# Optimization experiments

Measured on AMD Instinct MI355X. Metric: run time of the kernel, lower is better.

## Reference

```python
import jax, jax.numpy as jnp
import numpy as np

VOCAB = 32000
EMB = 256
HID = 512
SEQ = 512
SOS = 1  # word2vec key_to_index['<SOS>']; PAD assumed index 0 and never sampled


def setup_inputs() -> dict:
    key = jax.random.key(0)
    ks = jax.random.split(key, 8)
    k_lstm = 1.0 / np.sqrt(HID)
    k_out = 1.0 / np.sqrt(HID)
    return {
        # token ids in [2, VOCAB) so the PAD-skip branch never triggers
        "input_seq": jax.random.randint(ks[0], (1, SEQ), 2, VOCAB, dtype=jnp.int32),
        "h0": jnp.zeros((1, 1, HID), jnp.float32),
        "c0": jnp.zeros((1, 1, HID), jnp.float32),
        "embedding": jax.random.normal(ks[1], (VOCAB, EMB), jnp.float32) * 0.02,
        "W_ih": jax.random.uniform(ks[2], (4 * HID, EMB), jnp.float32, -k_lstm, k_lstm),
        "W_hh": jax.random.uniform(ks[3], (4 * HID, HID), jnp.float32, -k_lstm, k_lstm),
        "b_ih": jax.random.uniform(ks[4], (4 * HID,), jnp.float32, -k_lstm, k_lstm),
        "b_hh": jax.random.uniform(ks[5], (4 * HID,), jnp.float32, -k_lstm, k_lstm),
        "W_out": jax.random.uniform(ks[6], (VOCAB, HID), jnp.float32, -k_out, k_out),
        "b_out": jax.random.uniform(ks[7], (VOCAB,), jnp.float32, -k_out, k_out),
    }


def reference(input_seq, h0, c0, embedding, W_ih, W_hh, b_ih, b_hh, W_out, b_out):
    # tokens actually fed to the LSTM: <SOS> then the full teacher-forced sequence
    tokens = jnp.concatenate([jnp.array([SOS], jnp.int32), input_seq[0]])  # [S+1]
    emb = embedding[tokens]  # [S+1, E]
    bias = b_ih + b_hh

    def cell(carry, x_t):
        h, c = carry  # [H], [H]
        gates = W_ih @ x_t + W_hh @ h + bias  # [4H], torch gate order i,f,g,o
        i, f, g, o = jnp.split(gates, 4)
        i = jax.nn.sigmoid(i)
        f = jax.nn.sigmoid(f)
        g = jnp.tanh(g)
        o = jax.nn.sigmoid(o)
        c_new = f * c + i * g
        h_new = o * jnp.tanh(c_new)
        return (h_new, c_new), h_new

    (hT, cT), hs = jax.lax.scan(cell, (h0[0, 0], c0[0, 0]), emb)  # hs: [S+1, H]
    logits = hs @ W_out.T + b_out  # [S+1, V] (same math as per-step Linear + cat)
    outputs = logits[None]  # [1, S+1, V]
    return outputs, hT[None, None], cT[None, None]
```

## Files before the change

kernel.cpp:

```cpp
#include <hip/hip_runtime.h>
#include <cmath>

#define VOCAB 32000
#define EMB   256
#define HID   512
#define TLEN  513
#define G4    2048
#define NWG   32
#define SOS   1

typedef unsigned long long u64;
typedef unsigned int uivec4 __attribute__((ext_vector_type(4)));
typedef float f32x4 __attribute__((ext_vector_type(4)));
typedef short bf16x8 __attribute__((ext_vector_type(8)));

__device__ inline float fsig(float x)  { return __builtin_amdgcn_rcpf(1.f + __expf(-x)); }
__device__ inline float ftanh(float x) { return 1.f - 2.f * __builtin_amdgcn_rcpf(__expf(2.f * x) + 1.f); }
__device__ inline float fma4(f32x4 w, f32x4 h, float a) {
    return fmaf(w[0], h[0], fmaf(w[1], h[1], fmaf(w[2], h[2], fmaf(w[3], h[3], a))));
}

__device__ inline void bf16split(float f, short& h, short& l) {
    unsigned u = __float_as_uint(f);
    unsigned r = u + (0x7fffu + ((u >> 16) & 1u));
    unsigned hb = r & 0xffff0000u;
    h = (short)(hb >> 16);
    float res = f - __uint_as_float(hb);
    unsigned u2 = __float_as_uint(res);
    unsigned r2 = u2 + (0x7fffu + ((u2 >> 16) & 1u));
    l = (short)(r2 >> 16);
}

__global__ __launch_bounds__(256) void precompute_gates(
    const int* __restrict__ seq, const float* __restrict__ emb,
    const float* __restrict__ W_ih, const float* __restrict__ b_ih,
    const float* __restrict__ b_hh, float* __restrict__ Xg)
{
    __shared__ __align__(16) float ebuf[16][EMB];
    const int bt = blockIdx.x;
    const int br = blockIdx.y;
    const int tid = threadIdx.x;

    for (int tt = 0; tt < 16; ++tt) {
        int t = bt * 16 + tt;
        if (t < TLEN) {
            int tok = (t == 0) ? SOS : seq[t - 1];
            ebuf[tt][tid] = emb[(size_t)tok * EMB + tid];
        }
    }
    __syncthreads();

    const int row = br * 256 + tid;
    float acc[16];
#pragma unroll
    for (int tt = 0; tt < 16; ++tt) acc[tt] = 0.f;

    const float4* wp = (const float4*)(W_ih + (size_t)row * EMB);
#pragma unroll 4
    for (int k4 = 0; k4 < EMB / 4; ++k4) {
        float4 w = wp[k4];
#pragma unroll
        for (int tt = 0; tt < 16; ++tt) {
            float4 e = *(const float4*)&ebuf[tt][k4 * 4];
            acc[tt] = fmaf(w.x, e.x, fmaf(w.y, e.y, fmaf(w.z, e.z, fmaf(w.w, e.w, acc[tt]))));
        }
    }

    const float bias = b_ih[row] + b_hh[row];
    for (int tt = 0; tt < 16; ++tt) {
        int t = bt * 16 + tt;
        if (t < TLEN) Xg[(size_t)t * G4 + row] = acc[tt] + bias;
    }
}

__global__ __launch_bounds__(256, 1) void lstm_recurrence(
    const float* __restrict__ Xg, const float* __restrict__ W_hh,
    const float* __restrict__ h0, const float* __restrict__ c0,
    float* __restrict__ hs, u64* pk,
    float* __restrict__ out_hT, float* __restrict__ out_cT)
{
    __shared__ __align__(16) float hbuf[HID];
    __shared__ float pbuf[2][256];

    const int wg  = blockIdx.x;
    const int tid = threadIdx.x;
    const int wv  = tid >> 6;
    const int ln  = tid & 63;
    const int q   = ln >> 4;
    const int j   = ln & 15;
    const int row = q * HID + wg * 16 + j;

    f32x4 wreg[32];
    const f32x4* wp = (const f32x4*)(W_hh + (size_t)row * HID + wv * 128);
#pragma unroll
    for (int i = 0; i < 32; ++i) wreg[i] = wp[i];

    float c = (tid < 16) ? c0[wg * 16 + tid] : 0.f;
    {
        float2 h2 = *(const float2*)&h0[tid * 2];
        hbuf[tid * 2]     = h2.x;
        hbuf[tid * 2 + 1] = h2.y;
    }
    __syncthreads();

    for (int t = 0; t < TLEN; ++t) {
        float xg0 = 0.f, xg1 = 0.f, xg2 = 0.f, xg3 = 0.f;
        if (tid < 16) {
            const float* xp = Xg + (size_t)t * G4 + wg * 16 + tid;
            xg0 = xp[0]; xg1 = xp[512]; xg2 = xp[1024]; xg3 = xp[1536];
        }

        if (t > 0) {
            const unsigned tt = (unsigned)t;
            u64 sa = (u64)(uintptr_t)(pk + (size_t)(t & 1) * HID + 2 * tid);
            uivec4 r;
            do {
                asm volatile("global_load_dwordx4 %0, %1, off sc0 sc1\n\t"
                             "s_waitcnt vmcnt(0)" : "=v"(r) : "v"(sa));
            } while (r.y != tt || r.w != tt);
            hbuf[2 * tid]     = __uint_as_float(r.x);
            hbuf[2 * tid + 1] = __uint_as_float(r.z);
            asm volatile("s_waitcnt lgkmcnt(0)" ::: "memory");
        }

        float a0 = 0.f, a1 = 0.f, a2 = 0.f, a3 = 0.f;
        float a4 = 0.f, a5 = 0.f, a6 = 0.f, a7 = 0.f;
        const f32x4* hp = (const f32x4*)&hbuf[wv * 128];
#pragma unroll
        for (int i = 0; i < 32; i += 8) {
            a0 = fma4(wreg[i],     hp[i],     a0);
            a1 = fma4(wreg[i + 1], hp[i + 1], a1);
            a2 = fma4(wreg[i + 2], hp[i + 2], a2);
            a3 = fma4(wreg[i + 3], hp[i + 3], a3);
            a4 = fma4(wreg[i + 4], hp[i + 4], a4);
            a5 = fma4(wreg[i + 5], hp[i + 5], a5);
            a6 = fma4(wreg[i + 6], hp[i + 6], a6);
            a7 = fma4(wreg[i + 7], hp[i + 7], a7);
        }
        pbuf[t & 1][tid] = ((a0 + a1) + (a2 + a3)) + ((a4 + a5) + (a6 + a7));
        __syncthreads();

        if (tid < 16) {
            const float* pb = pbuf[t & 1];
            float gi = pb[tid]      + pb[64 + tid]  + pb[128 + tid] + pb[192 + tid] + xg0;
            float gf = pb[16 + tid] + pb[80 + tid]  + pb[144 + tid] + pb[208 + tid] + xg1;
            float gg = pb[32 + tid] + pb[96 + tid]  + pb[160 + tid] + pb[224 + tid] + xg2;
            float go = pb[48 + tid] + pb[112 + tid] + pb[176 + tid] + pb[240 + tid] + xg3;
            float i_ = fsig(gi);
            float f_ = fsig(gf);
            float g_ = ftanh(gg);
            float o_ = fsig(go);
            c = fmaf(f_, c, i_ * g_);
            float h_ = o_ * ftanh(c);
            if (t < TLEN - 1) {
                u64 word = ((u64)(unsigned)(t + 1) << 32) | (u64)__float_as_uint(h_);
                (void)__hip_atomic_exchange(
                    &pk[(size_t)((t + 1) & 1) * HID + wg * 16 + tid], word,
                    __ATOMIC_RELAXED, __HIP_MEMORY_SCOPE_AGENT);
            } else {
                out_hT[wg * 16 + tid] = h_;
                out_cT[wg * 16 + tid] = c;
            }
            hs[(size_t)t * HID + wg * 16 + tid] = h_;
        }
    }
}

#define GLDT 40

__global__ __launch_bounds__(256, 2) void out_gemm_mfma(
    const float* __restrict__ hs, const float* __restrict__ W_out,
    const float* __restrict__ b_out, float* __restrict__ out)
{
    __shared__ __align__(16) short Ah[128][GLDT];
    __shared__ __align__(16) short Al[128][GLDT];
    __shared__ __align__(16) short Bh[128][GLDT];
    __shared__ __align__(16) short Bl[128][GLDT];

    const int tb = blockIdx.x;
    const int vb = blockIdx.y;
    const int tid = threadIdx.x;
    const int w   = tid >> 6;
    const int l   = tid & 63;
    const int l15 = l & 15;
    const int lg  = l >> 4;
    const int m0 = tb * 128, n0 = vb * 128;

    const int sr = tid >> 1;
    const int kh = (tid & 1) * 16;

    f32x4 acc[2][8];
#pragma unroll
    for (int s = 0; s < 2; ++s)
#pragma unroll
        for (int cc = 0; cc < 8; ++cc) acc[s][cc] = (f32x4){0.f, 0.f, 0.f, 0.f};

    for (int k0 = 0; k0 < HID; k0 += 32) {
        {
            int trow = m0 + sr;
            float4 fa0 = make_float4(0.f,0.f,0.f,0.f), fa1 = fa0, fa2 = fa0, fa3 = fa0;
            if (trow < TLEN) {
                const float4* ap = (const float4*)(hs + (size_t)trow * HID + k0 + kh);
                fa0 = ap[0]; fa1 = ap[1]; fa2 = ap[2]; fa3 = ap[3];
            }
            float fv[16] = { fa0.x,fa0.y,fa0.z,fa0.w, fa1.x,fa1.y,fa1.z,fa1.w,
                             fa2.x,fa2.y,fa2.z,fa2.w, fa3.x,fa3.y,fa3.z,fa3.w };
#pragma unroll
            for (int g = 0; g < 2; ++g) {
                union { short s[8]; bf16x8 v; } ph, pl;
#pragma unroll
                for (int e = 0; e < 8; ++e) bf16split(fv[g * 8 + e], ph.s[e], pl.s[e]);
                *(bf16x8*)&Ah[sr][kh + 8 * g] = ph.v;
                *(bf16x8*)&Al[sr][kh + 8 * g] = pl.v;
            }
        }
        {
            const float4* bp = (const float4*)(W_out + (size_t)(n0 + sr) * HID + k0 + kh);
            float4 fb0 = bp[0], fb1 = bp[1], fb2 = bp[2], fb3 = bp[3];
            float fv[16] = { fb0.x,fb0.y,fb0.z,fb0.w, fb1.x,fb1.y,fb1.z,fb1.w,
                             fb2.x,fb2.y,fb2.z,fb2.w, fb3.x,fb3.y,fb3.z,fb3.w };
#pragma unroll
            for (int g = 0; g < 2; ++g) {
                union { short s[8]; bf16x8 v; } ph, pl;
#pragma unroll
                for (int e = 0; e < 8; ++e) bf16split(fv[g * 8 + e], ph.s[e], pl.s[e]);
                *(bf16x8*)&Bh[sr][kh + 8 * g] = ph.v;
                *(bf16x8*)&Bl[sr][kh + 8 * g] = pl.v;
            }
        }
        __syncthreads();

        bf16x8 ah[2], al2[2];
#pragma unroll
        for (int s = 0; s < 2; ++s) {
            ah[s]  = *(const bf16x8*)&Ah[32 * w + 16 * s + l15][8 * lg];
            al2[s] = *(const bf16x8*)&Al[32 * w + 16 * s + l15][8 * lg];
        }
#pragma unroll
        for (int cc = 0; cc < 8; ++cc) {
            bf16x8 bh = *(const bf16x8*)&Bh[16 * cc + l15][8 * lg];
            bf16x8 bl = *(const bf16x8*)&Bl[16 * cc + l15][8 * lg];
#pragma unroll
            for (int s = 0; s < 2; ++s) {
                acc[s][cc] = __builtin_amdgcn_mfma_f32_16x16x32_bf16(ah[s],  bh, acc[s][cc], 0, 0, 0);
                acc[s][cc] = __builtin_amdgcn_mfma_f32_16x16x32_bf16(ah[s],  bl, acc[s][cc], 0, 0, 0);
                acc[s][cc] = __builtin_amdgcn_mfma_f32_16x16x32_bf16(al2[s], bh, acc[s][cc], 0, 0, 0);
            }
        }
        __syncthreads();
    }

#pragma unroll
    for (int cc = 0; cc < 8; ++cc) {
        int col = n0 + 16 * cc + l15;
        float bo = b_out[col];
#pragma unroll
        for (int s = 0; s < 2; ++s) {
            int rbase = m0 + 32 * w + 16 * s + lg * 4;
#pragma unroll
            for (int r = 0; r < 4; ++r) {
                int trow = rbase + r;
                if (trow < TLEN) out[(size_t)trow * VOCAB + col] = acc[s][cc][r] + bo;
            }
        }
    }
}

extern "C" void kernel_launch(void* const* d_in, const int* in_sizes, int n_in,
                              void* d_out, int out_size, void* d_ws, size_t ws_size,
                              hipStream_t stream)
{
    const int*   seq   = (const int*)  d_in[0];
    const float* h0    = (const float*)d_in[1];
    const float* c0    = (const float*)d_in[2];
    const float* emb   = (const float*)d_in[3];
    const float* W_ih  = (const float*)d_in[4];
    const float* W_hh  = (const float*)d_in[5];
    const float* b_ih  = (const float*)d_in[6];
    const float* b_hh  = (const float*)d_in[7];
    const float* W_out = (const float*)d_in[8];
    const float* b_out = (const float*)d_in[9];

    float* out_logits = (float*)d_out;
    float* out_hT     = out_logits + (size_t)TLEN * VOCAB;
    float* out_cT     = out_hT + HID;

    float* Xg = (float*)d_ws;
    float* hs = Xg + (size_t)TLEN * G4;
    u64*   pk = (u64*)(hs + (size_t)TLEN * HID);

    (void)hipMemsetAsync(pk, 0, 2 * HID * sizeof(u64), stream);
    precompute_gates<<<dim3(33, 8), 256, 0, stream>>>(seq, emb, W_ih, b_ih, b_hh, Xg);
    lstm_recurrence<<<NWG, 256, 0, stream>>>(Xg, W_hh, h0, c0, hs, pk, out_hT, out_cT);
    out_gemm_mfma<<<dim3(5, 250), 256, 0, stream>>>(hs, W_out, b_out, out_logits);
}
```

Measured before the change: 957.4 us.

## Pre-split W_out into bf16 hi/lo in fused precompute kernel, feed MFMA gemm

Adds conversion blocks to the gate-precompute kernel that split W_out into bf16 high/low arrays in workspace. The recurrence also emits bf16 hi/lo copies of h. A new output GEMM loads the presplit operands directly instead of converting fp32 tiles inside the inner loop. The pk memset is folded into the fused kernel. The cost is extra memory traffic to write and reread the split weights.

```diff
diff --git a/kernel.cpp b/kernel.cpp
--- a/kernel.cpp
+++ b/kernel.cpp
@@ -8,6 +8,8 @@
 #define G4    2048
 #define NWG   32
 #define SOS   1
+#define NPRE  264
+#define NCVT  4000
 
 typedef unsigned long long u64;
 typedef unsigned int uivec4 __attribute__((ext_vector_type(4)));
@@ -31,15 +33,42 @@
     l = (short)(r2 >> 16);
 }
 
-__global__ __launch_bounds__(256) void precompute_gates(
+__global__ __launch_bounds__(256) void pre_fused(
     const int* __restrict__ seq, const float* __restrict__ emb,
     const float* __restrict__ W_ih, const float* __restrict__ b_ih,
-    const float* __restrict__ b_hh, float* __restrict__ Xg)
+    const float* __restrict__ b_hh, const float* __restrict__ W_out,
+    float* __restrict__ Xg, u64* pk,
+    short* __restrict__ Wh, short* __restrict__ Wl, int do_split)
 {
     __shared__ __align__(16) float ebuf[16][EMB];
-    const int bt = blockIdx.x;
-    const int br = blockIdx.y;
+    const int b   = blockIdx.x;
     const int tid = threadIdx.x;
+
+    if (b >= NPRE) {
+        if (!do_split) return;
+        if (b == NPRE) {
+#pragma unroll
+            for (int i = 0; i < 4; ++i) pk[tid + 256 * i] = 0;
+        }
+        const size_t base = (size_t)(b - NPRE) * 4096 + (size_t)tid * 16;
+        const float4* src = (const float4*)(W_out + base);
+        float4 f0 = src[0], f1 = src[1], f2 = src[2], f3 = src[3];
+        float fv[16] = { f0.x,f0.y,f0.z,f0.w, f1.x,f1.y,f1.z,f1.w,
+                         f2.x,f2.y,f2.z,f2.w, f3.x,f3.y,f3.z,f3.w };
+        union { short s[8]; bf16x8 v; } h0_, h1_, l0_, l1_;
+#pragma unroll
+        for (int e = 0; e < 8; ++e) bf16split(fv[e],     h0_.s[e], l0_.s[e]);
+#pragma unroll
+        for (int e = 0; e < 8; ++e) bf16split(fv[8 + e], h1_.s[e], l1_.s[e]);
+        *(bf16x8*)&Wh[base]     = h0_.v;
+        *(bf16x8*)&Wh[base + 8] = h1_.v;
+        *(bf16x8*)&Wl[base]     = l0_.v;
+        *(bf16x8*)&Wl[base + 8] = l1_.v;
+        return;
+    }
+
+    const int bt = b % 33;
+    const int br = b / 33;
 
     for (int tt = 0; tt < 16; ++tt) {
         int t = bt * 16 + tt;
@@ -76,8 +105,8 @@
 __global__ __launch_bounds__(256, 1) void lstm_recurrence(
     const float* __restrict__ Xg, const float* __restrict__ W_hh,
     const float* __restrict__ h0, const float* __restrict__ c0,
-    float* __restrict__ hs, u64* pk,
-    float* __restrict__ out_hT, float* __restrict__ out_cT)
+    float* __restrict__ hs, short* __restrict__ hs_h, short* __restrict__ hs_l,
+    u64* pk, float* __restrict__ out_hT, float* __restrict__ out_cT)
 {
     __shared__ __align__(16) float hbuf[HID];
     __shared__ float pbuf[2][256];
@@ -162,11 +191,104 @@
                 out_cT[wg * 16 + tid] = c;
             }
             hs[(size_t)t * HID + wg * 16 + tid] = h_;
+            short hh, hl; bf16split(h_, hh, hl);
+            hs_h[(size_t)t * HID + wg * 16 + tid] = hh;
+            hs_l[(size_t)t * HID + wg * 16 + tid] = hl;
         }
     }
 }
 
 #define GLDT 40
+
+__global__ __launch_bounds__(256, 2) void out_gemm_pre(
+    const short* __restrict__ hs_h, const short* __restrict__ hs_l,
+    const short* __restrict__ Wh, const short* __restrict__ Wl,
+    const float* __restrict__ b_out, float* __restrict__ out)
+{
+    __shared__ __align__(16) short Ah[128][GLDT];
+    __shared__ __align__(16) short Al[128][GLDT];
+    __shared__ __align__(16) short Bh[128][GLDT];
+    __shared__ __align__(16) short Bl[128][GLDT];
+
+    const int tb = blockIdx.x;
+    const int vb = blockIdx.y;
+    const int tid = threadIdx.x;
+    const int w   = tid >> 6;
+    const int l   = tid & 63;
+    const int l15 = l & 15;
+    const int lg  = l >> 4;
+    const int m0 = tb * 128, n0 = vb * 128;
+
+    const int sr = tid >> 1;
+    const int kh = (tid & 1) * 16;
+
+    f32x4 acc[2][8];
+#pragma unroll
+    for (int s = 0; s < 2; ++s)
+#pragma unroll
+        for (int cc = 0; cc < 8; ++cc) acc[s][cc] = (f32x4){0.f, 0.f, 0.f, 0.f};
+
+    for (int k0 = 0; k0 < HID; k0 += 32) {
+        {
+            int trow = m0 + sr;
+            bf16x8 z = (bf16x8)(short)0;
+            bf16x8 ah0 = z, ah1 = z, al0 = z, al1 = z;
+            if (trow < TLEN) {
+                const size_t o = (size_t)trow * HID + k0 + kh;
+                ah0 = *(const bf16x8*)&hs_h[o];
+                ah1 = *(const bf16x8*)&hs_h[o + 8];
+                al0 = *(const bf16x8*)&hs_l[o];
+                al1 = *(const bf16x8*)&hs_l[o + 8];
+            }
+            *(bf16x8*)&Ah[sr][kh]     = ah0;
+            *(bf16x8*)&Ah[sr][kh + 8] = ah1;
+            *(bf16x8*)&Al[sr][kh]     = al0;
+            *(bf16x8*)&Al[sr][kh + 8] = al1;
+        }
+        {
+            const size_t o = (size_t)(n0 + sr) * HID + k0 + kh;
+            *(bf16x8*)&Bh[sr][kh]     = *(const bf16x8*)&Wh[o];
+            *(bf16x8*)&Bh[sr][kh + 8] = *(const bf16x8*)&Wh[o + 8];
+            *(bf16x8*)&Bl[sr][kh]     = *(const bf16x8*)&Wl[o];
+            *(bf16x8*)&Bl[sr][kh + 8] = *(const bf16x8*)&Wl[o + 8];
+        }
+        __syncthreads();
+
+        bf16x8 ah[2], al2[2];
+#pragma unroll
+        for (int s = 0; s < 2; ++s) {
+            ah[s]  = *(const bf16x8*)&Ah[32 * w + 16 * s + l15][8 * lg];
+            al2[s] = *(const bf16x8*)&Al[32 * w + 16 * s + l15][8 * lg];
+        }
+#pragma unroll
+        for (int cc = 0; cc < 8; ++cc) {
+            bf16x8 bh = *(const bf16x8*)&Bh[16 * cc + l15][8 * lg];
+            bf16x8 bl = *(const bf16x8*)&Bl[16 * cc + l15][8 * lg];
+#pragma unroll
+            for (int s = 0; s < 2; ++s) {
+                acc[s][cc] = __builtin_amdgcn_mfma_f32_16x16x32_bf16(ah[s],  bh, acc[s][cc], 0, 0, 0);
+                acc[s][cc] = __builtin_amdgcn_mfma_f32_16x16x32_bf16(ah[s],  bl, acc[s][cc], 0, 0, 0);
+                acc[s][cc] = __builtin_amdgcn_mfma_f32_16x16x32_bf16(al2[s], bh, acc[s][cc], 0, 0, 0);
+            }
+        }
+        __syncthreads();
+    }
+
+#pragma unroll
+    for (int cc = 0; cc < 8; ++cc) {
+        int col = n0 + 16 * cc + l15;
+        float bo = b_out[col];
+#pragma unroll
+        for (int s = 0; s < 2; ++s) {
+            int rbase = m0 + 32 * w + 16 * s + lg * 4;
+#pragma unroll
+            for (int r = 0; r < 4; ++r) {
+                int trow = rbase + r;
+                if (trow < TLEN) out[(size_t)trow * VOCAB + col] = acc[s][cc][r] + bo;
+            }
+        }
+    }
+}
 
 __global__ __launch_bounds__(256, 2) void out_gemm_mfma(
     const float* __restrict__ hs, const float* __restrict__ W_out,
@@ -285,12 +407,30 @@
     float* out_hT     = out_logits + (size_t)TLEN * VOCAB;
     float* out_cT     = out_hT + HID;
 
-    float* Xg = (float*)d_ws;
-    float* hs = Xg + (size_t)TLEN * G4;
-    u64*   pk = (u64*)(hs + (size_t)TLEN * HID);
-
-    (void)hipMemsetAsync(pk, 0, 2 * HID * sizeof(u64), stream);
-    precompute_gates<<<dim3(33, 8), 256, 0, stream>>>(seq, emb, W_ih, b_ih, b_hh, Xg);
-    lstm_recurrence<<<NWG, 256, 0, stream>>>(Xg, W_hh, h0, c0, hs, pk, out_hT, out_cT);
-    out_gemm_mfma<<<dim3(5, 250), 256, 0, stream>>>(hs, W_out, b_out, out_logits);
-}
+    char*  base = (char*)d_ws;
+    float* Xg   = (float*)base;
+    float* hs   = (float*)(base + 4202496);
+    u64*   pk   = (u64*)  (base + 4202496 + 1050624);
+    short* hs_h = (short*)(base + 5261312);
+    short* hs_l = (short*)(base + 5261312 + 525312);
+    short* Wh   = (short*)(base + 6311936);
+    short* Wl   = (short*)(base + 6311936 + 32768000);
+    const size_t need_pre = 6311936ull + 2ull * 32768000ull;
+
+    const int use_pre = (ws_size >= need_pre) ? 1 : 0;
+
+    if (use_pre) {
+        pre_fused<<<NPRE + NCVT, 256, 0, stream>>>(seq, emb, W_ih, b_ih, b_hh, W_out,
+                                                   Xg, pk, Wh, Wl, 1);
+        lstm_recurrence<<<NWG, 256, 0, stream>>>(Xg, W_hh, h0, c0, hs, hs_h, hs_l, pk,
+                                                 out_hT, out_cT);
+        out_gemm_pre<<<dim3(5, 250), 256, 0, stream>>>(hs_h, hs_l, Wh, Wl, b_out, out_logits);
+    } else {
+        (void)hipMemsetAsync(pk, 0, 2 * HID * sizeof(u64), stream);
+        pre_fused<<<NPRE, 256, 0, stream>>>(seq, emb, W_ih, b_ih, b_hh, W_out,
+                                            Xg, pk, hs_h , hs_l , 0);
+        lstm_recurrence<<<NWG, 256, 0, stream>>>(Xg, W_hh, h0, c0, hs, hs_h, hs_l, pk,
+                                                 out_hT, out_cT);
+        out_gemm_mfma<<<dim3(5, 250), 256, 0, stream>>>(hs, W_out, b_out, out_logits);
+    }
+}
```

After: 981.5 us. 1.03x slower.

## Fuse LSTM recurrence and output GEMM into persistent kernel with flag-gated tiles

Applied to the files above, without the earlier changes.

Merges the recurrence and the output-projection GEMM into one persistent launch of 256 workgroups. 32 workgroups run the recurrence and publish each h row as pre-split bf16 hi/lo tagged with a step counter. The remaining 224 pull GEMM tiles from an atomic work queue and spin on per-128-row ready counters and tags. This lets the vocabulary GEMM overlap the serial recurrence, drops the memset, and removes the second bf16 split of A. The risks are forward-progress assumptions (all 256 blocks must be co-resident, which is forced by LDS padding), spin traffic that may slow the latency-bound recurrence, and the last row being handled by a scalar path.

```diff
diff --git a/kernel.cpp b/kernel.cpp
--- a/kernel.cpp
+++ b/kernel.cpp
@@ -7,10 +7,15 @@
 #define TLEN  513
 #define G4    2048
 #define NWG   32
+#define NWORK 224
+#define GRID_MEGA 256
+#define NTILE_V 250
+#define NTILES  (5 * NTILE_V)
 #define SOS   1
 
 typedef unsigned long long u64;
 typedef unsigned int uivec4 __attribute__((ext_vector_type(4)));
+typedef unsigned int uivec2 __attribute__((ext_vector_type(2)));
 typedef float f32x4 __attribute__((ext_vector_type(4)));
 typedef short bf16x8 __attribute__((ext_vector_type(8)));
 
@@ -34,13 +39,20 @@
 __global__ __launch_bounds__(256) void precompute_gates(
     const int* __restrict__ seq, const float* __restrict__ emb,
     const float* __restrict__ W_ih, const float* __restrict__ b_ih,
-    const float* __restrict__ b_hh, float* __restrict__ Xg)
+    const float* __restrict__ b_hh, float* __restrict__ Xg,
+    u64* pk, int* flags)
 {
     __shared__ __align__(16) float ebuf[16][EMB];
     const int bt = blockIdx.x;
     const int br = blockIdx.y;
     const int tid = threadIdx.x;
 
+    if (bt == 0 && br == 0) {
+#pragma unroll
+        for (int i = 0; i < 4; ++i) pk[tid + 256 * i] = 0;
+        if (tid < 16) flags[tid] = 0;
+    }
+
     for (int tt = 0; tt < 16; ++tt) {
         int t = bt * 16 + tt;
         if (t < TLEN) {
@@ -73,194 +85,274 @@
     }
 }
 
-__global__ __launch_bounds__(256, 1) void lstm_recurrence(
+#define GLDT 40
+
+__global__ __launch_bounds__(256, 1) void mega(
     const float* __restrict__ Xg, const float* __restrict__ W_hh,
     const float* __restrict__ h0, const float* __restrict__ c0,
-    float* __restrict__ hs, u64* pk,
-    float* __restrict__ out_hT, float* __restrict__ out_cT)
-{
-    __shared__ __align__(16) float hbuf[HID];
-    __shared__ float pbuf[2][256];
-
-    const int wg  = blockIdx.x;
-    const int tid = threadIdx.x;
-    const int wv  = tid >> 6;
-    const int ln  = tid & 63;
-    const int q   = ln >> 4;
-    const int j   = ln & 15;
-    const int row = q * HID + wg * 16 + j;
-
-    f32x4 wreg[32];
-    const f32x4* wp = (const f32x4*)(W_hh + (size_t)row * HID + wv * 128);
-#pragma unroll
-    for (int i = 0; i < 32; ++i) wreg[i] = wp[i];
-
-    float c = (tid < 16) ? c0[wg * 16 + tid] : 0.f;
-    {
-        float2 h2 = *(const float2*)&h0[tid * 2];
-        hbuf[tid * 2]     = h2.x;
-        hbuf[tid * 2 + 1] = h2.y;
-    }
-    __syncthreads();
-
-    for (int t = 0; t < TLEN; ++t) {
-        float xg0 = 0.f, xg1 = 0.f, xg2 = 0.f, xg3 = 0.f;
-        if (tid < 16) {
-            const float* xp = Xg + (size_t)t * G4 + wg * 16 + tid;
-            xg0 = xp[0]; xg1 = xp[512]; xg2 = xp[1024]; xg3 = xp[1536];
-        }
-
-        if (t > 0) {
-            const unsigned tt = (unsigned)t;
-            u64 sa = (u64)(uintptr_t)(pk + (size_t)(t & 1) * HID + 2 * tid);
-            uivec4 r;
-            do {
-                asm volatile("global_load_dwordx4 %0, %1, off sc0 sc1\n\t"
-                             "s_waitcnt vmcnt(0)" : "=v"(r) : "v"(sa));
-            } while (r.y != tt || r.w != tt);
-            hbuf[2 * tid]     = __uint_as_float(r.x);
-            hbuf[2 * tid + 1] = __uint_as_float(r.z);
-            asm volatile("s_waitcnt lgkmcnt(0)" ::: "memory");
-        }
-
-        float a0 = 0.f, a1 = 0.f, a2 = 0.f, a3 = 0.f;
-        float a4 = 0.f, a5 = 0.f, a6 = 0.f, a7 = 0.f;
-        const f32x4* hp = (const f32x4*)&hbuf[wv * 128];
-#pragma unroll
-        for (int i = 0; i < 32; i += 8) {
-            a0 = fma4(wreg[i],     hp[i],     a0);
-            a1 = fma4(wreg[i + 1], hp[i + 1], a1);
-            a2 = fma4(wreg[i + 2], hp[i + 2], a2);
-            a3 = fma4(wreg[i + 3], hp[i + 3], a3);
-            a4 = fma4(wreg[i + 4], hp[i + 4], a4);
-            a5 = fma4(wreg[i + 5], hp[i + 5], a5);
-            a6 = fma4(wreg[i + 6], hp[i + 6], a6);
-            a7 = fma4(wreg[i + 7], hp[i + 7], a7);
-        }
-        pbuf[t & 1][tid] = ((a0 + a1) + (a2 + a3)) + ((a4 + a5) + (a6 + a7));
-        __syncthreads();
-
-        if (tid < 16) {
-            const float* pb = pbuf[t & 1];
-            float gi = pb[tid]      + pb[64 + tid]  + pb[128 + tid] + pb[192 + tid] + xg0;
-            float gf = pb[16 + tid] + pb[80 + tid]  + pb[144 + tid] + pb[208 + tid] + xg1;
-            float gg = pb[32 + tid] + pb[96 + tid]  + pb[160 + tid] + pb[224 + tid] + xg2;
-            float go = pb[48 + tid] + pb[112 + tid] + pb[176 + tid] + pb[240 + tid] + xg3;
-            float i_ = fsig(gi);
-            float f_ = fsig(gf);
-            float g_ = ftanh(gg);
-            float o_ = fsig(go);
-            c = fmaf(f_, c, i_ * g_);
-            float h_ = o_ * ftanh(c);
-            if (t < TLEN - 1) {
-                u64 word = ((u64)(unsigned)(t + 1) << 32) | (u64)__float_as_uint(h_);
-                (void)__hip_atomic_exchange(
-                    &pk[(size_t)((t + 1) & 1) * HID + wg * 16 + tid], word,
-                    __ATOMIC_RELAXED, __HIP_MEMORY_SCOPE_AGENT);
-            } else {
-                out_hT[wg * 16 + tid] = h_;
-                out_cT[wg * 16 + tid] = c;
-            }
-            hs[(size_t)t * HID + wg * 16 + tid] = h_;
-        }
-    }
-}
-
-#define GLDT 40
-
-__global__ __launch_bounds__(256, 2) void out_gemm_mfma(
-    const float* __restrict__ hs, const float* __restrict__ W_out,
-    const float* __restrict__ b_out, float* __restrict__ out)
+    const float* __restrict__ W_out, const float* __restrict__ b_out,
+    u64* pk, u64* hs_t, int* flags,
+    float* __restrict__ out, float* __restrict__ out_hT, float* __restrict__ out_cT)
 {
     __shared__ __align__(16) short Ah[128][GLDT];
     __shared__ __align__(16) short Al[128][GLDT];
     __shared__ __align__(16) short Bh[128][GLDT];
     __shared__ __align__(16) short Bl[128][GLDT];
-
-    const int tb = blockIdx.x;
-    const int vb = blockIdx.y;
+    __shared__ __align__(16) float hbuf[HID];
+    __shared__ float pbuf[2][256];
+    __shared__ int s_idx;
+    __shared__ char lds_pad[40960];
+
     const int tid = threadIdx.x;
+    int* ready = flags;
+    int* wq    = flags + 8;
+
+    if (blockIdx.x < NWG) {
+        lds_pad[0] = 0;
+        const int wg  = blockIdx.x;
+        const int wv  = tid >> 6;
+        const int ln  = tid & 63;
+        const int q   = ln >> 4;
+        const int j   = ln & 15;
+        const int row = q * HID + wg * 16 + j;
+
+        f32x4 wreg[32];
+        const f32x4* wp = (const f32x4*)(W_hh + (size_t)row * HID + wv * 128);
+#pragma unroll
+        for (int i = 0; i < 32; ++i) wreg[i] = wp[i];
+
+        float c = (tid < 16) ? c0[wg * 16 + tid] : 0.f;
+        {
+            float2 h2 = *(const float2*)&h0[tid * 2];
+            hbuf[tid * 2]     = h2.x;
+            hbuf[tid * 2 + 1] = h2.y;
+        }
+        __syncthreads();
+
+        for (int t = 0; t < TLEN; ++t) {
+            float xg0 = 0.f, xg1 = 0.f, xg2 = 0.f, xg3 = 0.f;
+            if (tid < 16) {
+                const float* xp = Xg + (size_t)t * G4 + wg * 16 + tid;
+                xg0 = xp[0]; xg1 = xp[512]; xg2 = xp[1024]; xg3 = xp[1536];
+            }
+
+            if (t > 0) {
+                const unsigned tt = (unsigned)t;
+                u64 sa = (u64)(uintptr_t)(pk + (size_t)(t & 1) * HID + 2 * tid);
+                uivec4 r;
+                do {
+                    asm volatile("global_load_dwordx4 %0, %1, off sc0 sc1\n\t"
+                                 "s_waitcnt vmcnt(0)" : "=v"(r) : "v"(sa));
+                } while (r.y != tt || r.w != tt);
+                hbuf[2 * tid]     = __uint_as_float(r.x);
+                hbuf[2 * tid + 1] = __uint_as_float(r.z);
+                asm volatile("s_waitcnt lgkmcnt(0)" ::: "memory");
+            }
+
+            float a0 = 0.f, a1 = 0.f, a2 = 0.f, a3 = 0.f;
+            float a4 = 0.f, a5 = 0.f, a6 = 0.f, a7 = 0.f;
+            const f32x4* hp = (const f32x4*)&hbuf[wv * 128];
+#pragma unroll
+            for (int i = 0; i < 32; i += 8) {
+                a0 = fma4(wreg[i],     hp[i],     a0);
+                a1 = fma4(wreg[i + 1], hp[i + 1], a1);
+                a2 = fma4(wreg[i + 2], hp[i + 2], a2);
+                a3 = fma4(wreg[i + 3], hp[i + 3], a3);
+                a4 = fma4(wreg[i + 4], hp[i + 4], a4);
+                a5 = fma4(wreg[i + 5], hp[i + 5], a5);
+                a6 = fma4(wreg[i + 6], hp[i + 6], a6);
+                a7 = fma4(wreg[i + 7], hp[i + 7], a7);
+            }
+            pbuf[t & 1][tid] = ((a0 + a1) + (a2 + a3)) + ((a4 + a5) + (a6 + a7));
+            __syncthreads();
+
+            if (tid < 16) {
+                const float* pb = pbuf[t & 1];
+                float gi = pb[tid]      + pb[64 + tid]  + pb[128 + tid] + pb[192 + tid] + xg0;
+                float gf = pb[16 + tid] + pb[80 + tid]  + pb[144 + tid] + pb[208 + tid] + xg1;
+                float gg = pb[32 + tid] + pb[96 + tid]  + pb[160 + tid] + pb[224 + tid] + xg2;
+                float go = pb[48 + tid] + pb[112 + tid] + pb[176 + tid] + pb[240 + tid] + xg3;
+                float i_ = fsig(gi);
+                float f_ = fsig(gf);
+                float g_ = ftanh(gg);
+                float o_ = fsig(go);
+                c = fmaf(f_, c, i_ * g_);
+                float h_ = o_ * ftanh(c);
+
+                if (t < TLEN - 1) {
+                    u64 word = ((u64)(unsigned)(t + 1) << 32) | (u64)__float_as_uint(h_);
+                    (void)__hip_atomic_exchange(
+                        &pk[(size_t)((t + 1) & 1) * HID + wg * 16 + tid], word,
+                        __ATOMIC_RELAXED, __HIP_MEMORY_SCOPE_AGENT);
+                }
+                short hh, hl; bf16split(h_, hh, hl);
+                u64 aw = ((u64)(unsigned)(t + 1) << 32)
+                       | (u64)((((unsigned)(unsigned short)hh) << 16) | (unsigned)(unsigned short)hl);
+                __hip_atomic_store(&hs_t[(size_t)t * HID + wg * 16 + tid], aw,
+                                   __ATOMIC_RELAXED, __HIP_MEMORY_SCOPE_AGENT);
+                if (t == TLEN - 1) {
+                    out_hT[wg * 16 + tid] = h_;
+                    out_cT[wg * 16 + tid] = c;
+                }
+                if (tid == 0) {
+                    if (t == 127 || t == 255 || t == 383 || t == 511)
+                        __hip_atomic_fetch_add(&ready[t >> 7], 1,
+                                               __ATOMIC_RELAXED, __HIP_MEMORY_SCOPE_AGENT);
+                    if (t == TLEN - 1)
+                        __hip_atomic_fetch_add(&ready[4], 1,
+                                               __ATOMIC_RELAXED, __HIP_MEMORY_SCOPE_AGENT);
+                }
+            }
+        }
+        return;
+    }
+
     const int w   = tid >> 6;
     const int l   = tid & 63;
     const int l15 = l & 15;
     const int lg  = l >> 4;
-    const int m0 = tb * 128, n0 = vb * 128;
-
-    const int sr = tid >> 1;
-    const int kh = (tid & 1) * 16;
-
-    f32x4 acc[2][8];
-#pragma unroll
-    for (int s = 0; s < 2; ++s)
-#pragma unroll
-        for (int cc = 0; cc < 8; ++cc) acc[s][cc] = (f32x4){0.f, 0.f, 0.f, 0.f};
-
-    for (int k0 = 0; k0 < HID; k0 += 32) {
-        {
-            int trow = m0 + sr;
-            float4 fa0 = make_float4(0.f,0.f,0.f,0.f), fa1 = fa0, fa2 = fa0, fa3 = fa0;
-            if (trow < TLEN) {
-                const float4* ap = (const float4*)(hs + (size_t)trow * HID + k0 + kh);
-                fa0 = ap[0]; fa1 = ap[1]; fa2 = ap[2]; fa3 = ap[3];
-            }
-            float fv[16] = { fa0.x,fa0.y,fa0.z,fa0.w, fa1.x,fa1.y,fa1.z,fa1.w,
-                             fa2.x,fa2.y,fa2.z,fa2.w, fa3.x,fa3.y,fa3.z,fa3.w };
-#pragma unroll
-            for (int g = 0; g < 2; ++g) {
-                union { short s[8]; bf16x8 v; } ph, pl;
-#pragma unroll
-                for (int e = 0; e < 8; ++e) bf16split(fv[g * 8 + e], ph.s[e], pl.s[e]);
-                *(bf16x8*)&Ah[sr][kh + 8 * g] = ph.v;
-                *(bf16x8*)&Al[sr][kh + 8 * g] = pl.v;
-            }
-        }
-        {
-            const float4* bp = (const float4*)(W_out + (size_t)(n0 + sr) * HID + k0 + kh);
-            float4 fb0 = bp[0], fb1 = bp[1], fb2 = bp[2], fb3 = bp[3];
-            float fv[16] = { fb0.x,fb0.y,fb0.z,fb0.w, fb1.x,fb1.y,fb1.z,fb1.w,
-                             fb2.x,fb2.y,fb2.z,fb2.w, fb3.x,fb3.y,fb3.z,fb3.w };
-#pragma unroll
-            for (int g = 0; g < 2; ++g) {
-                union { short s[8]; bf16x8 v; } ph, pl;
-#pragma unroll
-                for (int e = 0; e < 8; ++e) bf16split(fv[g * 8 + e], ph.s[e], pl.s[e]);
-                *(bf16x8*)&Bh[sr][kh + 8 * g] = ph.v;
-                *(bf16x8*)&Bl[sr][kh + 8 * g] = pl.v;
-            }
-        }
+    const int sr  = tid >> 1;
+    const int kh  = (tid & 1) * 16;
+
+    for (;;) {
+        if (tid == 0)
+            s_idx = __hip_atomic_fetch_add(wq, 1, __ATOMIC_RELAXED, __HIP_MEMORY_SCOPE_AGENT);
         __syncthreads();
-
-        bf16x8 ah[2], al2[2];
-#pragma unroll
-        for (int s = 0; s < 2; ++s) {
-            ah[s]  = *(const bf16x8*)&Ah[32 * w + 16 * s + l15][8 * lg];
-            al2[s] = *(const bf16x8*)&Al[32 * w + 16 * s + l15][8 * lg];
-        }
+        const int idx = s_idx;
+        __syncthreads();
+        if (idx >= NTILES) break;
+        const int tb = idx / NTILE_V;
+        const int vb = idx % NTILE_V;
+
+        if (tid == 0) {
+            while (__hip_atomic_load(&ready[tb], __ATOMIC_RELAXED,
+                                     __HIP_MEMORY_SCOPE_AGENT) < NWG)
+                __builtin_amdgcn_s_sleep(32);
+        }
+        __syncthreads();
+
+        if (tb == 4) {
+            float* hrow = (float*)&Ah[0][0];
+            for (int jj = tid; jj < HID; jj += 256) {
+                u64 ad = (u64)(uintptr_t)(hs_t + (size_t)512 * HID + jj);
+                uivec2 r2;
+                do {
+                    asm volatile("global_load_dwordx2 %0, %1, off sc0 sc1\n\t"
+                                 "s_waitcnt vmcnt(0)" : "=v"(r2) : "v"(ad));
+                } while (r2.y != 513u);
+                hrow[jj] = __uint_as_float(r2.x & 0xffff0000u)
+                         + __uint_as_float((r2.x & 0xffffu) << 16);
+            }
+            __syncthreads();
+            if (tid < 128) {
+                int col = vb * 128 + tid;
+                const float4* wr = (const float4*)(W_out + (size_t)col * HID);
+                float d0 = 0.f, d1 = 0.f, d2 = 0.f, d3 = 0.f;
+#pragma unroll 4
+                for (int k = 0; k < HID / 16; ++k) {
+                    float4 w0 = wr[4*k], w1 = wr[4*k+1], w2 = wr[4*k+2], w3 = wr[4*k+3];
+                    const float* hp = hrow + 16 * k;
+                    d0 = fmaf(w0.x, hp[0],  fmaf(w0.y, hp[1],  fmaf(w0.z, hp[2],  fmaf(w0.w, hp[3],  d0))));
+                    d1 = fmaf(w1.x, hp[4],  fmaf(w1.y, hp[5],  fmaf(w1.z, hp[6],  fmaf(w1.w, hp[7],  d1))));
+                    d2 = fmaf(w2.x, hp[8],  fmaf(w2.y, hp[9],  fmaf(w2.z, hp[10], fmaf(w2.w, hp[11], d2))));
+                    d3 = fmaf(w3.x, hp[12], fmaf(w3.y, hp[13], fmaf(w3.z, hp[14], fmaf(w3.w, hp[15], d3))));
+                }
+                out[(size_t)512 * VOCAB + col] = ((d0 + d1) + (d2 + d3)) + b_out[col];
+            }
+            __syncthreads();
+            continue;
+        }
+
+        const int m0 = tb * 128, n0 = vb * 128;
+        f32x4 acc[2][8];
+#pragma unroll
+        for (int s = 0; s < 2; ++s)
+#pragma unroll
+            for (int cc = 0; cc < 8; ++cc) acc[s][cc] = (f32x4){0.f, 0.f, 0.f, 0.f};
+
+        for (int k0 = 0; k0 < HID; k0 += 32) {
+            {
+                uivec4 rr[8];
+                u64 ad[8];
+                unsigned tg[8];
+#pragma unroll
+                for (int it = 0; it < 8; ++it) {
+                    int li = it * 256 + tid;
+                    int m  = li >> 4;
+                    int kp = li & 15;
+                    ad[it] = (u64)(uintptr_t)(hs_t + (size_t)(m0 + m) * HID + k0 + kp * 2);
+                    tg[it] = (unsigned)(m0 + m + 1);
+                }
+                bool done = false;
+                while (!done) {
+#pragma unroll
+                    for (int it = 0; it < 8; ++it)
+                        asm volatile("global_load_dwordx4 %0, %1, off sc0 sc1"
+                                     : "=v"(rr[it]) : "v"(ad[it]));
+                    asm volatile("s_waitcnt vmcnt(0)");
+                    done = true;
+#pragma unroll
+                    for (int it = 0; it < 8; ++it)
+                        if (rr[it].y != tg[it] || rr[it].w != tg[it]) done = false;
+                }
+#pragma unroll
+                for (int it = 0; it < 8; ++it) {
+                    int li = it * 256 + tid;
+                    int m  = li >> 4;
+                    int kp = li & 15;
+                    Ah[m][kp * 2]     = (short)(rr[it].x >> 16);
+                    Al[m][kp * 2]     = (short)(rr[it].x & 0xffffu);
+                    Ah[m][kp * 2 + 1] = (short)(rr[it].z >> 16);
+                    Al[m][kp * 2 + 1] = (short)(rr[it].z & 0xffffu);
+                }
+            }
+            {
+                const float4* bp = (const float4*)(W_out + (size_t)(n0 + sr) * HID + k0 + kh);
+                float4 fb0 = bp[0], fb1 = bp[1], fb2 = bp[2], fb3 = bp[3];
+                float fv[16] = { fb0.x,fb0.y,fb0.z,fb0.w, fb1.x,fb1.y,fb1.z,fb1.w,
+                                 fb2.x,fb2.y,fb2.z,fb2.w, fb3.x,fb3.y,fb3.z,fb3.w };
+#pragma unroll
+                for (int g = 0; g < 2; ++g) {
+                    union { short s[8]; bf16x8 v; } ph, pl;
+#pragma unroll
+                    for (int e = 0; e < 8; ++e) bf16split(fv[g * 8 + e], ph.s[e], pl.s[e]);
+                    *(bf16x8*)&Bh[sr][kh + 8 * g] = ph.v;
+                    *(bf16x8*)&Bl[sr][kh + 8 * g] = pl.v;
+                }
+            }
+            __syncthreads();
+
+            bf16x8 ah[2], al2[2];
+#pragma unroll
+            for (int s = 0; s < 2; ++s) {
+                ah[s]  = *(const bf16x8*)&Ah[32 * w + 16 * s + l15][8 * lg];
+                al2[s] = *(const bf16x8*)&Al[32 * w + 16 * s + l15][8 * lg];
+            }
+#pragma unroll
+            for (int cc = 0; cc < 8; ++cc) {
+                bf16x8 bh = *(const bf16x8*)&Bh[16 * cc + l15][8 * lg];
+                bf16x8 bl = *(const bf16x8*)&Bl[16 * cc + l15][8 * lg];
+#pragma unroll
+                for (int s = 0; s < 2; ++s) {
+                    acc[s][cc] = __builtin_amdgcn_mfma_f32_16x16x32_bf16(ah[s],  bh, acc[s][cc], 0, 0, 0);
+                    acc[s][cc] = __builtin_amdgcn_mfma_f32_16x16x32_bf16(ah[s],  bl, acc[s][cc], 0, 0, 0);
+                    acc[s][cc] = __builtin_amdgcn_mfma_f32_16x16x32_bf16(al2[s], bh, acc[s][cc], 0, 0, 0);
+                }
+            }
+            __syncthreads();
+        }
+
 #pragma unroll
         for (int cc = 0; cc < 8; ++cc) {
-            bf16x8 bh = *(const bf16x8*)&Bh[16 * cc + l15][8 * lg];
-            bf16x8 bl = *(const bf16x8*)&Bl[16 * cc + l15][8 * lg];
+            int col = n0 + 16 * cc + l15;
+            float bo = b_out[col];
 #pragma unroll
             for (int s = 0; s < 2; ++s) {
-                acc[s][cc] = __builtin_amdgcn_mfma_f32_16x16x32_bf16(ah[s],  bh, acc[s][cc], 0, 0, 0);
-                acc[s][cc] = __builtin_amdgcn_mfma_f32_16x16x32_bf16(ah[s],  bl, acc[s][cc], 0, 0, 0);
-                acc[s][cc] = __builtin_amdgcn_mfma_f32_16x16x32_bf16(al2[s], bh, acc[s][cc], 0, 0, 0);
-            }
-        }
-        __syncthreads();
-    }
-
-#pragma unroll
-    for (int cc = 0; cc < 8; ++cc) {
-        int col = n0 + 16 * cc + l15;
-        float bo = b_out[col];
-#pragma unroll
-        for (int s = 0; s < 2; ++s) {
-            int rbase = m0 + 32 * w + 16 * s + lg * 4;
-#pragma unroll
-            for (int r = 0; r < 4; ++r) {
-                int trow = rbase + r;
-                if (trow < TLEN) out[(size_t)trow * VOCAB + col] = acc[s][cc][r] + bo;
+                int rbase = m0 + 32 * w + 16 * s + lg * 4;
+#pragma unroll
+                for (int r = 0; r < 4; ++r) {
+                    out[(size_t)(rbase + r) * VOCAB + col] = acc[s][cc][r] + bo;
+                }
             }
         }
     }
@@ -285,12 +377,15 @@
     float* out_hT     = out_logits + (size_t)TLEN * VOCAB;
     float* out_cT     = out_hT + HID;
 
-    float* Xg = (float*)d_ws;
-    float* hs = Xg + (size_t)TLEN * G4;
-    u64*   pk = (u64*)(hs + (size_t)TLEN * HID);
-
-    (void)hipMemsetAsync(pk, 0, 2 * HID * sizeof(u64), stream);
-    precompute_gates<<<dim3(33, 8), 256, 0, stream>>>(seq, emb, W_ih, b_ih, b_hh, Xg);
-    lstm_recurrence<<<NWG, 256, 0, stream>>>(Xg, W_hh, h0, c0, hs, pk, out_hT, out_cT);
-    out_gemm_mfma<<<dim3(5, 250), 256, 0, stream>>>(hs, W_out, b_out, out_logits);
-}
+    char*  base = (char*)d_ws;
+    float* Xg   = (float*)base;
+    u64*   pk   = (u64*)(base + 4202496);
+    u64*   hs_t = (u64*)(base + 4202496 + 8192);
+    int*   flags= (int*)(base + 4202496 + 8192 + 2101248);
+
+    precompute_gates<<<dim3(33, 8), 256, 0, stream>>>(seq, emb, W_ih, b_ih, b_hh,
+                                                      Xg, pk, flags);
+    mega<<<GRID_MEGA, 256, 0, stream>>>(Xg, W_hh, h0, c0, W_out, b_out,
+                                        pk, hs_t, flags,
+                                        out_logits, out_hT, out_cT);
+}
```

Measured after the change: 957.5 us. No clear change (+0.0%).
